# Kernel optimization log

Measured on AMD Instinct MI355X. Metric: run time of the kernel, lower is better.

## Reference

```python
import jax, jax.numpy as jnp
import numpy as np

EMBED_DIM = 1024
NUM_HEADS = 16
HEAD_DIM = EMBED_DIM // NUM_HEADS


def setup_inputs() -> dict:
    key = jax.random.key(0)
    k1, k2, k3, k4, k5 = jax.random.split(key, 5)
    B, S, D = 4, 2048, EMBED_DIM
    scale = 1.0 / np.sqrt(D)
    qkv = jax.random.normal(k1, (B, S, D), dtype=jnp.float32)
    W_in = jax.random.uniform(k2, (D, 3 * D), dtype=jnp.float32, minval=-scale, maxval=scale)
    b_in = jax.random.uniform(k3, (3 * D,), dtype=jnp.float32, minval=-scale, maxval=scale)
    W_out = jax.random.uniform(k4, (D, D), dtype=jnp.float32, minval=-scale, maxval=scale)
    b_out = jax.random.uniform(k5, (D,), dtype=jnp.float32, minval=-scale, maxval=scale)
    return {"qkv": qkv, "W_in": W_in, "b_in": b_in, "W_out": W_out, "b_out": b_out}


def reference(qkv, W_in, b_in, W_out, b_out):
    B, S, D = qkv.shape
    H, hd = NUM_HEADS, HEAD_DIM
    proj = qkv @ W_in + b_in                      # [B, S, 3D]
    q, k, v = jnp.split(proj, 3, axis=-1)         # each [B, S, D]
    # reshape to heads: [B, H, S, hd]
    q = q.reshape(B, S, H, hd).transpose(0, 2, 1, 3)
    k = k.reshape(B, S, H, hd).transpose(0, 2, 1, 3)
    v = v.reshape(B, S, H, hd).transpose(0, 2, 1, 3)
    scores = jnp.einsum('bhqd,bhkd->bhqk', q, k) / jnp.sqrt(jnp.float32(hd))
    attn = jax.nn.softmax(scores, axis=-1)        # dropout=0.0 -> identity
    ctx = jnp.einsum('bhqk,bhkd->bhqd', attn, v)  # [B, H, S, hd]
    ctx = ctx.transpose(0, 2, 1, 3).reshape(B, S, D)
    return ctx @ W_out + b_out
```

## Files before the change

### kernel.cpp

```cpp
#include <hip/hip_runtime.h>


typedef __bf16 bf16;
typedef __bf16 bf16x4 __attribute__((ext_vector_type(4)));
typedef __bf16 bf16x8 __attribute__((ext_vector_type(8)));
typedef float f32x4 __attribute__((ext_vector_type(4)));

typedef const __attribute__((address_space(1))) void* gas1p;
typedef __attribute__((address_space(3))) void* las3p;
#define GLD16(g, l) __builtin_amdgcn_global_load_lds((gas1p)(g), (las3p)(l), 16, 0, 0)

#if __has_builtin(__builtin_amdgcn_exp2f)
#define EXP2(x) __builtin_amdgcn_exp2f(x)
#else
#define EXP2(x) exp2f(x)
#endif

__device__ __forceinline__ f32x4 mfma16(bf16x8 a, bf16x8 b, f32x4 c) {
  return __builtin_amdgcn_mfma_f32_16x16x32_bf16(a, b, c, 0, 0, 0);
}

__global__ void cast_kernel(const float* __restrict__ in, bf16* __restrict__ out, int n) {
  int i = (blockIdx.x * 256 + threadIdx.x) * 4;
  if (i < n) {
    float4 v = *(const float4*)(in + i);
    bf16x4 o;
    o[0] = (bf16)v.x; o[1] = (bf16)v.y; o[2] = (bf16)v.z; o[3] = (bf16)v.w;
    *(bf16x4*)(out + i) = o;
  }
}

__global__ void transpose_cast_kernel(const float* __restrict__ in, bf16* __restrict__ out,
                                      int R, int C) {
  __shared__ float tile[32][33];
  int c0 = blockIdx.x * 32, r0 = blockIdx.y * 32;
  int tx = threadIdx.x, ty = threadIdx.y;
#pragma unroll
  for (int i = 0; i < 4; ++i)
    tile[ty + i * 8][tx] = in[(size_t)(r0 + ty + i * 8) * C + c0 + tx];
  __syncthreads();
#pragma unroll
  for (int i = 0; i < 4; ++i)
    out[(size_t)(c0 + ty + i * 8) * R + r0 + tx] = (bf16)tile[tx][ty + i * 8];
}

__global__ __launch_bounds__(256, 2) void gemm1_kernel(
    const bf16* __restrict__ A, const bf16* __restrict__ Bt, const float* __restrict__ bias,
    bf16* __restrict__ Qo, bf16* __restrict__ Ko, bf16* __restrict__ Vo) {
  __shared__ __align__(16) char sA[128 * 64 * 2];
  __shared__ __align__(16) char sB[128 * 64 * 2];
  const int tid = threadIdx.x, lane = tid & 63, wave = tid >> 6, quad = lane >> 4;
  const int m0 = blockIdx.y * 128, n0 = blockIdx.x * 128;
  const int wm = (wave >> 1) * 64, wn = (wave & 1) * 64;
  f32x4 acc[4][4] = {};

  for (int kt = 0; kt < 1024; kt += 64) {
    __syncthreads();
#pragma unroll
    for (int i = 0; i < 4; ++i) {
      int chunk = i * 256 + tid;
      int row = chunk >> 3;
      int cs = (chunk & 7) ^ (row & 7);
      GLD16(A + (size_t)(m0 + row) * 1024 + kt + cs * 8, sA + chunk * 16);
      GLD16(Bt + (size_t)(n0 + row) * 1024 + kt + cs * 8, sB + chunk * 16);
    }
    __syncthreads();
#pragma unroll
    for (int ks = 0; ks < 2; ++ks) {
      bf16x8 af[4], bfr[4];
#pragma unroll
      for (int t = 0; t < 4; ++t) {
        int ra = wm + t * 16 + (lane & 15);
        af[t] = *(const bf16x8*)(sA + ra * 128 + ((ks * 4 + quad) ^ (ra & 7)) * 16);
        int rb = wn + t * 16 + (lane & 15);
        bfr[t] = *(const bf16x8*)(sB + rb * 128 + ((ks * 4 + quad) ^ (rb & 7)) * 16);
      }
#pragma unroll
      for (int mt = 0; mt < 4; ++mt)
#pragma unroll
        for (int nt = 0; nt < 4; ++nt)
          acc[mt][nt] = mfma16(af[mt], bfr[nt], acc[mt][nt]);
    }
  }

  const int region = n0 >> 10;
#pragma unroll
  for (int nt = 0; nt < 4; ++nt) {
    int n = n0 + wn + nt * 16 + (lane & 15);
    float bv = bias[n];
    int ncol = n & 1023;
    int h = ncol >> 6, d = ncol & 63;
#pragma unroll
    for (int mt = 0; mt < 4; ++mt) {
      int gm = m0 + wm + mt * 16 + quad * 4;
      int bb = gm >> 11, s = gm & 2047;
      if (region == 2) {
        bf16x4 pk;
#pragma unroll
        for (int r = 0; r < 4; ++r) pk[r] = (bf16)(acc[mt][nt][r] + bv);
        *(bf16x4*)(Vo + ((size_t)((bb * 16 + h) * 64 + d)) * 2048 + s) = pk;
      } else {
        bf16* dst = (region == 0) ? Qo : Ko;
        float scl = (region == 0) ? 0.18033688f : 1.0f;
#pragma unroll
        for (int r = 0; r < 4; ++r)
          dst[((size_t)((bb * 16 + h) * 2048) + s + r) * 64 + d] =
              (bf16)((acc[mt][nt][r] + bv) * scl);
      }
    }
  }
}

__global__ __launch_bounds__(256, 4) void flash_kernel(
    const bf16* __restrict__ Q, const bf16* __restrict__ K, const bf16* __restrict__ Vt,
    bf16* __restrict__ ctx) {
  const int n = blockIdx.x;
  const int bh = (n & 7) * 8 + (n >> 7);
  const int qt = (n >> 3) & 15;
  const int b = bh >> 4, h = bh & 15;
  const int tid = threadIdx.x, lane = tid & 63, wave = tid >> 6, quad = lane >> 4;

  __shared__ __align__(16) char sK[128 * 64 * 2];
  __shared__ __align__(16) char sV[64 * 128 * 2];
  __shared__ __align__(16) char sP[4][32 * 32 * 2];

  const size_t hb = (size_t)bh * 2048 * 64;
  const int q0 = qt * 128;

#pragma unroll
  for (int i = 0; i < 4; ++i) {
    int chunk = i * 256 + tid;
    int row = chunk >> 3;
    int cs = (chunk & 7) ^ (row & 7);
    GLD16(Q + hb + (size_t)(q0 + row) * 64 + cs * 8, sK + chunk * 16);
  }
  __syncthreads();
  bf16x8 qf[2][2];
#pragma unroll
  for (int j = 0; j < 2; ++j)
#pragma unroll
    for (int ksd = 0; ksd < 2; ++ksd) {
      int row = wave * 32 + j * 16 + (lane & 15);
      qf[j][ksd] = *(const bf16x8*)(sK + row * 128 + ((ksd * 4 + quad) ^ (row & 7)) * 16);
    }

  f32x4 ctxa[2][4] = {};
  float l[2] = {0.f, 0.f};
  char* pw = sP[wave];

  for (int kv0 = 0; kv0 < 2048; kv0 += 128) {
    __syncthreads();
#pragma unroll
    for (int i = 0; i < 4; ++i) {
      int chunk = i * 256 + tid;
      int row = chunk >> 3;
      int cs = (chunk & 7) ^ (row & 7);
      GLD16(K + hb + (size_t)(kv0 + row) * 64 + cs * 8, sK + chunk * 16);
    }
#pragma unroll
    for (int i = 0; i < 4; ++i) {
      int chunk = i * 256 + tid;
      int row = chunk >> 4;
      int cs = (chunk & 15) ^ (row & 7);
      GLD16(Vt + hb + (size_t)row * 2048 + kv0 + cs * 8, sV + chunk * 16);
    }
    __syncthreads();

#pragma unroll
    for (int kq = 0; kq < 4; ++kq) {
      f32x4 st[2][2] = {};
#pragma unroll
      for (int ksd = 0; ksd < 2; ++ksd) {
        bf16x8 kf[2];
#pragma unroll
        for (int ii = 0; ii < 2; ++ii) {
          int row = kq * 32 + ii * 16 + (lane & 15);
          kf[ii] = *(const bf16x8*)(sK + row * 128 + ((ksd * 4 + quad) ^ (row & 7)) * 16);
        }
#pragma unroll
        for (int ii = 0; ii < 2; ++ii)
#pragma unroll
          for (int j = 0; j < 2; ++j)
            st[ii][j] = mfma16(kf[ii], qf[j][ksd], st[ii][j]);
      }
#pragma unroll
      for (int ii = 0; ii < 2; ++ii)
#pragma unroll
        for (int j = 0; j < 2; ++j) {
          f32x4 p;
#pragma unroll
          for (int r = 0; r < 4; ++r) {
            p[r] = EXP2(st[ii][j][r]);
            l[j] += p[r];
          }
          bf16x4 pk;
#pragma unroll
          for (int r = 0; r < 4; ++r) pk[r] = (bf16)p[r];
          int q = j * 16 + (lane & 15);
          int chunk = ii * 2 + (quad >> 1);
          *(bf16x4*)(pw + q * 64 + ((chunk ^ (q & 3)) * 16) + (quad & 1) * 8) = pk;
        }
      bf16x8 pf[2], vf[4];
#pragma unroll
      for (int mt = 0; mt < 2; ++mt) {
        int q = mt * 16 + (lane & 15);
        pf[mt] = *(const bf16x8*)(pw + q * 64 + ((quad ^ (q & 3)) * 16));
      }
#pragma unroll
      for (int nd = 0; nd < 4; ++nd) {
        int row = nd * 16 + (lane & 15);
        vf[nd] = *(const bf16x8*)(sV + row * 256 + (((kq * 4 + quad) ^ (row & 7)) * 16));
      }
#pragma unroll
      for (int mt = 0; mt < 2; ++mt)
#pragma unroll
        for (int nd = 0; nd < 4; ++nd)
          ctxa[mt][nd] = mfma16(pf[mt], vf[nd], ctxa[mt][nd]);
    }
  }

#pragma unroll
  for (int j = 0; j < 2; ++j) {
    l[j] += __shfl_xor(l[j], 16);
    l[j] += __shfl_xor(l[j], 32);
  }
#pragma unroll
  for (int mt = 0; mt < 2; ++mt)
#pragma unroll
    for (int r = 0; r < 4; ++r) {
      float lsh = __shfl(l[mt], quad * 4 + r);
      float rl = __builtin_amdgcn_rcpf(lsh);
      int srow = q0 + wave * 32 + mt * 16 + quad * 4 + r;
#pragma unroll
      for (int nd = 0; nd < 4; ++nd) {
        int col = h * 64 + nd * 16 + (lane & 15);
        ctx[((size_t)(b * 2048 + srow)) * 1024 + col] = (bf16)(ctxa[mt][nd][r] * rl);
      }
    }
}

__global__ __launch_bounds__(256, 2) void gemm2_kernel(
    const bf16* __restrict__ A, const bf16* __restrict__ Bt, const float* __restrict__ bias,
    float* __restrict__ Out) {
  __shared__ __align__(16) char sA[128 * 64 * 2];
  __shared__ __align__(16) char sB[128 * 64 * 2];
  const int tid = threadIdx.x, lane = tid & 63, wave = tid >> 6, quad = lane >> 4;
  const int m0 = blockIdx.y * 128, n0 = blockIdx.x * 128;
  const int wm = (wave >> 1) * 64, wn = (wave & 1) * 64;
  f32x4 acc[4][4] = {};

  for (int kt = 0; kt < 1024; kt += 64) {
    __syncthreads();
#pragma unroll
    for (int i = 0; i < 4; ++i) {
      int chunk = i * 256 + tid;
      int row = chunk >> 3;
      int cs = (chunk & 7) ^ (row & 7);
      GLD16(A + (size_t)(m0 + row) * 1024 + kt + cs * 8, sA + chunk * 16);
      GLD16(Bt + (size_t)(n0 + row) * 1024 + kt + cs * 8, sB + chunk * 16);
    }
    __syncthreads();
#pragma unroll
    for (int ks = 0; ks < 2; ++ks) {
      bf16x8 af[4], bfr[4];
#pragma unroll
      for (int t = 0; t < 4; ++t) {
        int ra = wm + t * 16 + (lane & 15);
        af[t] = *(const bf16x8*)(sA + ra * 128 + ((ks * 4 + quad) ^ (ra & 7)) * 16);
        int rb = wn + t * 16 + (lane & 15);
        bfr[t] = *(const bf16x8*)(sB + rb * 128 + ((ks * 4 + quad) ^ (rb & 7)) * 16);
      }
#pragma unroll
      for (int mt = 0; mt < 4; ++mt)
#pragma unroll
        for (int nt = 0; nt < 4; ++nt)
          acc[mt][nt] = mfma16(af[mt], bfr[nt], acc[mt][nt]);
    }
  }

#pragma unroll
  for (int nt = 0; nt < 4; ++nt) {
    int n = n0 + wn + nt * 16 + (lane & 15);
    float bv = bias[n];
#pragma unroll
    for (int mt = 0; mt < 4; ++mt) {
      int gm = m0 + wm + mt * 16 + quad * 4;
#pragma unroll
      for (int r = 0; r < 4; ++r)
        Out[(size_t)(gm + r) * 1024 + n] = acc[mt][nt][r] + bv;
    }
  }
}

extern "C" void kernel_launch(void* const* d_in, const int* in_sizes, int n_in,
                              void* d_out, int out_size, void* d_ws, size_t ws_size,
                              hipStream_t stream) {
  const float* qkv   = (const float*)d_in[0];
  const float* W_in  = (const float*)d_in[1];
  const float* b_in  = (const float*)d_in[2];
  const float* W_out = (const float*)d_in[3];
  const float* b_out = (const float*)d_in[4];
  float* out = (float*)d_out;

  bf16* Xb    = (bf16*)d_ws;
  bf16* WtIn  = Xb + 8388608;
  bf16* WtOut = WtIn + 3145728;
  bf16* Qb    = WtOut + 1048576;
  bf16* Kb    = Qb + 8388608;
  bf16* Vtb   = Kb + 8388608;
  bf16* Ctx   = Xb;

  cast_kernel<<<8192, 256, 0, stream>>>(qkv, Xb, 8388608);
  transpose_cast_kernel<<<dim3(96, 32), dim3(32, 8), 0, stream>>>(W_in, WtIn, 1024, 3072);
  transpose_cast_kernel<<<dim3(32, 32), dim3(32, 8), 0, stream>>>(W_out, WtOut, 1024, 1024);
  gemm1_kernel<<<dim3(24, 64), 256, 0, stream>>>(Xb, WtIn, b_in, Qb, Kb, Vtb);
  flash_kernel<<<1024, 256, 0, stream>>>(Qb, Kb, Vtb, Ctx);
  gemm2_kernel<<<dim3(8, 64), 256, 0, stream>>>(Ctx, WtOut, b_out, out);
}
```

Baseline: 278.2 us.

## Double-buffer K tiles in LDS and load V fragments directly from global

Flash attention now double-buffers K tiles in shared memory, prefetching the next KV block while the current one is computed, with one barrier per iteration instead of two. V tiles no longer go through LDS: each lane loads its bf16x8 V^T fragments straight from global memory into registers at the start of each sub-block. This aims to hide global latency and cut LDS traffic and barriers. The trade-off is uncoalesced-ish direct global loads of V that every wave repeats, plus a prefetch-then-barrier ordering that relies on GLD completion before the end-of-iteration sync.

```diff
diff --git a/kernel.cpp b/kernel.cpp
--- a/kernel.cpp
+++ b/kernel.cpp
@@ -120,8 +120,7 @@
   const int b = bh >> 4, h = bh & 15;
   const int tid = threadIdx.x, lane = tid & 63, wave = tid >> 6, quad = lane >> 4;
 
-  __shared__ __align__(16) char sK[128 * 64 * 2];
-  __shared__ __align__(16) char sV[64 * 128 * 2];
+  __shared__ __align__(16) char sK[2][128 * 64 * 2];
   __shared__ __align__(16) char sP[4][32 * 32 * 2];
 
   const size_t hb = (size_t)bh * 2048 * 64;
@@ -132,7 +131,8 @@
     int chunk = i * 256 + tid;
     int row = chunk >> 3;
     int cs = (chunk & 7) ^ (row & 7);
-    GLD16(Q + hb + (size_t)(q0 + row) * 64 + cs * 8, sK + chunk * 16);
+    GLD16(Q + hb + (size_t)(q0 + row) * 64 + cs * 8, sK[1] + chunk * 16);
+    GLD16(K + hb + (size_t)row * 64 + cs * 8, sK[0] + chunk * 16);
   }
   __syncthreads();
   bf16x8 qf[2][2];
@@ -141,33 +141,37 @@
 #pragma unroll
     for (int ksd = 0; ksd < 2; ++ksd) {
       int row = wave * 32 + j * 16 + (lane & 15);
-      qf[j][ksd] = *(const bf16x8*)(sK + row * 128 + ((ksd * 4 + quad) ^ (row & 7)) * 16);
-    }
+      qf[j][ksd] = *(const bf16x8*)(sK[1] + row * 128 + ((ksd * 4 + quad) ^ (row & 7)) * 16);
+    }
+  __syncthreads();
+
+  const bf16* vbase = Vt + hb + (size_t)(lane & 15) * 2048 + quad * 8;
 
   f32x4 ctxa[2][4] = {};
   float l[2] = {0.f, 0.f};
   char* pw = sP[wave];
 
-  for (int kv0 = 0; kv0 < 2048; kv0 += 128) {
-    __syncthreads();
-#pragma unroll
-    for (int i = 0; i < 4; ++i) {
-      int chunk = i * 256 + tid;
-      int row = chunk >> 3;
-      int cs = (chunk & 7) ^ (row & 7);
-      GLD16(K + hb + (size_t)(kv0 + row) * 64 + cs * 8, sK + chunk * 16);
-    }
-#pragma unroll
-    for (int i = 0; i < 4; ++i) {
-      int chunk = i * 256 + tid;
-      int row = chunk >> 4;
-      int cs = (chunk & 15) ^ (row & 7);
-      GLD16(Vt + hb + (size_t)row * 2048 + kv0 + cs * 8, sV + chunk * 16);
-    }
-    __syncthreads();
+  for (int it = 0; it < 16; ++it) {
+    const int kv0 = it * 128;
+    if (it < 15) {
+      char* nb = sK[(it + 1) & 1];
+#pragma unroll
+      for (int i = 0; i < 4; ++i) {
+        int chunk = i * 256 + tid;
+        int row = chunk >> 3;
+        int cs = (chunk & 7) ^ (row & 7);
+        GLD16(K + hb + (size_t)(kv0 + 128 + row) * 64 + cs * 8, nb + chunk * 16);
+      }
+    }
+    const char* cb = sK[it & 1];
 
 #pragma unroll
     for (int kq = 0; kq < 4; ++kq) {
+      bf16x8 vf[4];
+#pragma unroll
+      for (int nd = 0; nd < 4; ++nd)
+        vf[nd] = *(const bf16x8*)(vbase + (size_t)nd * 32768 + kv0 + kq * 32);
+
       f32x4 st[2][2] = {};
 #pragma unroll
       for (int ksd = 0; ksd < 2; ++ksd) {
@@ -175,7 +179,7 @@
 #pragma unroll
         for (int ii = 0; ii < 2; ++ii) {
           int row = kq * 32 + ii * 16 + (lane & 15);
-          kf[ii] = *(const bf16x8*)(sK + row * 128 + ((ksd * 4 + quad) ^ (row & 7)) * 16);
+          kf[ii] = *(const bf16x8*)(cb + row * 128 + ((ksd * 4 + quad) ^ (row & 7)) * 16);
         }
 #pragma unroll
         for (int ii = 0; ii < 2; ++ii)
@@ -200,23 +204,19 @@
           int chunk = ii * 2 + (quad >> 1);
           *(bf16x4*)(pw + q * 64 + ((chunk ^ (q & 3)) * 16) + (quad & 1) * 8) = pk;
         }
-      bf16x8 pf[2], vf[4];
+      bf16x8 pf[2];
 #pragma unroll
       for (int mt = 0; mt < 2; ++mt) {
         int q = mt * 16 + (lane & 15);
         pf[mt] = *(const bf16x8*)(pw + q * 64 + ((quad ^ (q & 3)) * 16));
       }
 #pragma unroll
-      for (int nd = 0; nd < 4; ++nd) {
-        int row = nd * 16 + (lane & 15);
-        vf[nd] = *(const bf16x8*)(sV + row * 256 + (((kq * 4 + quad) ^ (row & 7)) * 16));
-      }
-#pragma unroll
       for (int mt = 0; mt < 2; ++mt)
 #pragma unroll
         for (int nd = 0; nd < 4; ++nd)
           ctxa[mt][nd] = mfma16(pf[mt], vf[nd], ctxa[mt][nd]);
     }
+    __syncthreads();
   }
 
 #pragma unroll
```

Result: slower. 495.7 us (+78.2%).
